# Kernel tuning notes

Measured on AMD Instinct MI355X. Metric: run time of the kernel, lower is better.

## Reference

```python
import math
import jax, jax.numpy as jnp
import numpy as np

B, LD, LE = 8, 512, 512
D, H, DK, F, L, V = 1024, 16, 64, 4096, 3, 32000
EPS = 1e-5
NEG = -1000000000.0


def setup_inputs() -> dict:
    key = jax.random.key(0)
    ks = jax.random.split(key, 16)
    s = 0.02
    dec_inputs = jax.random.randint(ks[0], (B, LD), 0, V)
    # causal mask: True = masked out (matches masked_fill semantics)
    self_mask = jnp.broadcast_to(jnp.triu(jnp.ones((LD, LD), bool), k=1), (B, LD, LD))
    enc_output = jax.random.normal(ks[1], (B, LE, D), jnp.float32)
    encoder_mask = jnp.zeros((B, LD, LE), bool)  # no encoder padding
    embed = jax.random.normal(ks[2], (V, D), jnp.float32) * s
    # sinusoidal positional encoding, pe[:LD]
    pos = jnp.arange(LD, dtype=jnp.float32)[:, None]
    div = jnp.exp(jnp.arange(0, D, 2, dtype=jnp.float32) * (-math.log(10000.0) / D))
    pe = jnp.zeros((LD, D), jnp.float32)
    pe = pe.at[:, 0::2].set(jnp.sin(pos * div)).at[:, 1::2].set(jnp.cos(pos * div))
    # per-layer params; axis 1 of attn params: 0=self-attn, 1=enc-dec attn
    wq = jax.random.normal(ks[3], (L, 2, D, D), jnp.float32) * s
    wk = jax.random.normal(ks[4], (L, 2, D, D), jnp.float32) * s
    wv = jax.random.normal(ks[5], (L, 2, D, D), jnp.float32) * s
    wo = jax.random.normal(ks[6], (L, 2, D, D), jnp.float32) * s
    bq = jnp.zeros((L, 2, D), jnp.float32)
    bk = jnp.zeros((L, 2, D), jnp.float32)
    bv = jnp.zeros((L, 2, D), jnp.float32)
    bo = jnp.zeros((L, 2, D), jnp.float32)
    ffn_w1 = jax.random.normal(ks[7], (L, F, D), jnp.float32) * s
    ffn_b1 = jnp.zeros((L, F), jnp.float32)
    ffn_w2 = jax.random.normal(ks[8], (L, D, F), jnp.float32) * s
    ffn_b2 = jnp.zeros((L, D), jnp.float32)
    ln_g = jnp.ones((L, 3, D), jnp.float32)   # norm1/2/3 gains
    ln_b = jnp.zeros((L, 3, D), jnp.float32)  # norm1/2/3 biases
    return dict(dec_inputs=dec_inputs, self_mask=self_mask, enc_output=enc_output,
                encoder_mask=encoder_mask, embed=embed, pe=pe,
                wq=wq, bq=bq, wk=wk, bk=bk, wv=wv, bv=bv, wo=wo, bo=bo,
                ffn_w1=ffn_w1, ffn_b1=ffn_b1, ffn_w2=ffn_w2, ffn_b2=ffn_b2,
                ln_g=ln_g, ln_b=ln_b)


def _ln(x, g, b):
    m = jnp.mean(x, axis=-1, keepdims=True)
    v = jnp.mean((x - m) ** 2, axis=-1, keepdims=True)
    return (x - m) * jax.lax.rsqrt(v + EPS) * g + b


def _mha(qi, ki, vi, mask, wq, bq, wk, bk, wv, bv, wo, bo):
    Bq, Lq, _ = qi.shape
    Lk = ki.shape[1]
    Q = (qi @ wq.T + bq).reshape(Bq, Lq, H, DK).transpose(0, 2, 1, 3)
    K = (ki @ wk.T + bk).reshape(Bq, Lk, H, DK).transpose(0, 2, 1, 3)
    Vv = (vi @ wv.T + bv).reshape(Bq, Lk, H, DK).transpose(0, 2, 1, 3)
    scores = jnp.einsum('bhqd,bhkd->bhqk', Q, K) / math.sqrt(DK)
    scores = jnp.where(mask[:, None, :, :], NEG, scores)
    attn = jax.nn.softmax(scores, axis=-1)
    ctx = jnp.einsum('bhqk,bhkd->bhqd', attn, Vv)
    ctx = ctx.transpose(0, 2, 1, 3).reshape(Bq, Lq, H * DK)
    return ctx @ wo.T + bo


def reference(dec_inputs, self_mask, enc_output, encoder_mask, embed, pe,
              wq, bq, wk, bk, wv, bv, wo, bo,
              ffn_w1, ffn_b1, ffn_w2, ffn_b2, ln_g, ln_b):
    x = embed[dec_inputs] * math.sqrt(D) + pe[None, :, :]
    for l in range(L):
        h = _ln(x, ln_g[l, 0], ln_b[l, 0])
        a = _mha(h, h, h, self_mask,
                 wq[l, 0], bq[l, 0], wk[l, 0], bk[l, 0], wv[l, 0], bv[l, 0], wo[l, 0], bo[l, 0])
        x = x + a
        h = _ln(x, ln_g[l, 1], ln_b[l, 1])
        c = _mha(h, enc_output, enc_output, encoder_mask,
                 wq[l, 1], bq[l, 1], wk[l, 1], bk[l, 1], wv[l, 1], bv[l, 1], wo[l, 1], bo[l, 1])
        x = x + c
        h = _ln(x, ln_g[l, 2], ln_b[l, 2])
        f = jax.nn.relu(h @ ffn_w1[l].T + ffn_b1[l]) @ ffn_w2[l].T + ffn_b2[l]
        # faithful quirk of the source: residual is the cross-attn output, not x
        x = c + f
    return x
```

## Files before the change

### kernel.cpp

```cpp
#include <hip/hip_runtime.h>
#include <hip/hip_bf16.h>

using bf16x8 = __attribute__((ext_vector_type(8))) short;
using f32x4  = __attribute__((ext_vector_type(4))) float;
using u16x4  = __attribute__((ext_vector_type(4))) unsigned short;

#define DEVI static __device__ __forceinline__

DEVI unsigned short f2b(float f) {
  unsigned int u = __float_as_uint(f);
  u += 0x7FFFu + ((u >> 16) & 1u);
  return (unsigned short)(u >> 16);
}

DEVI void gload16(const unsigned short* g, unsigned short* l) {
  __builtin_amdgcn_global_load_lds(
      (const __attribute__((address_space(1))) unsigned int*)g,
      (__attribute__((address_space(3))) unsigned int*)l, 16, 0, 0);
}

DEVI float wred_max16(float v) {
#pragma unroll
  for (int m = 1; m < 16; m <<= 1) v = fmaxf(v, __shfl_xor(v, m, 64));
  return v;
}
DEVI float wred_sum16(float v) {
#pragma unroll
  for (int m = 1; m < 16; m <<= 1) v += __shfl_xor(v, m, 64);
  return v;
}


__global__ void cvt_kernel(const float* __restrict__ in,
                           unsigned short* __restrict__ out, int n4) {
  int i = blockIdx.x * blockDim.x + threadIdx.x;
  const int stride = gridDim.x * blockDim.x;
  for (; i < n4; i += stride) {
    const float4 v = ((const float4*)in)[i];
    u16x4 o;
    o[0] = f2b(v.x); o[1] = f2b(v.y); o[2] = f2b(v.z); o[3] = f2b(v.w);
    ((u16x4*)out)[i] = o;
  }
}

__global__ void pack_w(const float* __restrict__ s0,
                       const float* __restrict__ s1,
                       const float* __restrict__ s2,
                       int sub, unsigned short* __restrict__ dst, int nm) {
  const int r = blockIdx.x;
  const int m = blockIdx.y;
  const int l = blockIdx.z;
  const float* src = (m == 0 ? s0 : m == 1 ? s1 : s2)
                   + (size_t)(l * 2 + sub) * 1048576 + (size_t)r * 1024;
  unsigned short* d = dst + ((size_t)(l * nm + m) * 1024 + r) * 1024;
  const int col = threadIdx.x * 4;
  const float4 v = *(const float4*)(src + col);
  u16x4 o;
  o[0] = f2b(v.x); o[1] = f2b(v.y); o[2] = f2b(v.z); o[3] = f2b(v.w);
  *(u16x4*)(d + col) = o;
}

__global__ void pack_bias(const float* __restrict__ s0,
                          const float* __restrict__ s1,
                          const float* __restrict__ s2,
                          int sub, float* __restrict__ dst, int nm) {
  const int m = blockIdx.x, l = blockIdx.y;
  const float* src = (m == 0 ? s0 : m == 1 ? s1 : s2) + (size_t)(l * 2 + sub) * 1024;
  float* d = dst + ((size_t)l * nm + m) * 1024;
  const int i = threadIdx.x * 4;
  *(float4*)(d + i) = *(const float4*)(src + i);
}

__global__ void embed_kernel(const int* __restrict__ ids,
                             const float* __restrict__ emb,
                             const float* __restrict__ pe,
                             float* __restrict__ x) {
  const int row = blockIdx.x;
  const int t = row & 511;
  const int col = threadIdx.x * 4;
  const int id = ids[row];
  const float4 e = *(const float4*)(emb + (size_t)id * 1024 + col);
  const float4 p = *(const float4*)(pe + (size_t)t * 1024 + col);
  float4 o;
  o.x = e.x * 32.f + p.x; o.y = e.y * 32.f + p.y;
  o.z = e.z * 32.f + p.z; o.w = e.w * 32.f + p.w;
  *(float4*)(x + (size_t)row * 1024 + col) = o;
}

__global__ void ln_kernel(const float* __restrict__ x,
                          const float* __restrict__ g,
                          const float* __restrict__ b,
                          unsigned short* __restrict__ out) {
  const int row = blockIdx.x;
  const int l = threadIdx.x;
  const float4* xr = (const float4*)(x + (size_t)row * 1024);
  float4 v[4];
  float s = 0.f;
#pragma unroll
  for (int i = 0; i < 4; ++i) {
    v[i] = xr[l * 4 + i];
    s += v[i].x + v[i].y + v[i].z + v[i].w;
  }
#pragma unroll
  for (int m = 1; m < 64; m <<= 1) s += __shfl_xor(s, m, 64);
  const float mean = s * (1.f / 1024.f);
  float vs = 0.f;
#pragma unroll
  for (int i = 0; i < 4; ++i) {
    float dx = v[i].x - mean, dy = v[i].y - mean, dz = v[i].z - mean, dw = v[i].w - mean;
    vs += dx * dx + dy * dy + dz * dz + dw * dw;
  }
#pragma unroll
  for (int m = 1; m < 64; m <<= 1) vs += __shfl_xor(vs, m, 64);
  const float inv = rsqrtf(vs * (1.f / 1024.f) + 1e-5f);
#pragma unroll
  for (int i = 0; i < 4; ++i) {
    const int col = l * 16 + i * 4;
    const float4 gg = *(const float4*)(g + col);
    const float4 bb = *(const float4*)(b + col);
    u16x4 o;
    o[0] = f2b((v[i].x - mean) * inv * gg.x + bb.x);
    o[1] = f2b((v[i].y - mean) * inv * gg.y + bb.y);
    o[2] = f2b((v[i].z - mean) * inv * gg.z + bb.z);
    o[3] = f2b((v[i].w - mean) * inv * gg.w + bb.w);
    *(u16x4*)(out + (size_t)row * 1024 + col) = o;
  }
}

__global__ void vt_kernel(const unsigned short* __restrict__ Vsrc, int vsd,
                          unsigned short* __restrict__ Vt) {
  __shared__ alignas(16) unsigned short t[64][72];
  const int tt = blockIdx.x;
  const int h  = blockIdx.y;
  const int b  = blockIdx.z;
  const int tid = threadIdx.x;
  const int r  = tid >> 2;
  const int ch = tid & 3;
  const unsigned short* src =
      Vsrc + (size_t)(b * 512 + tt * 64 + r) * vsd + (size_t)h * 64 + ch * 16;
  const bf16x8 v0 = *(const bf16x8*)src;
  const bf16x8 v1 = *(const bf16x8*)(src + 8);
#pragma unroll
  for (int j = 0; j < 8; ++j) {
    t[ch * 16 + j][r]     = (unsigned short)v0[j];
    t[ch * 16 + 8 + j][r] = (unsigned short)v1[j];
  }
  __syncthreads();
  const int d  = tid >> 2;
  const int tp = tid & 3;
  unsigned short* dst = Vt + (((size_t)(b * 16 + h) * 64 + d) * 512) + tt * 64 + tp * 16;
  *(bf16x8*)dst       = *(const bf16x8*)&t[d][tp * 16];
  *(bf16x8*)(dst + 8) = *(const bf16x8*)&t[d][tp * 16 + 8];
}


template<int EPI>
__global__ __launch_bounds__(512, 2) void gemm256(
    const unsigned short* __restrict__ A,
    const unsigned short* __restrict__ Bw,
    const float* __restrict__ bias,
    int N, unsigned short* __restrict__ out0) {
  constexpr int K = 1024, NK = 16;
  __shared__ alignas(16) unsigned short As0[256 * 64];
  __shared__ alignas(16) unsigned short As1[256 * 64];
  __shared__ alignas(16) unsigned short As2[256 * 64];
  __shared__ alignas(16) unsigned short Bs0[128 * 64];
  __shared__ alignas(16) unsigned short Bs1[128 * 64];
  __shared__ alignas(16) unsigned short Bs2[128 * 64];
  const int tid = threadIdx.x;
  const int lane = tid & 63;
  const int wave = tid >> 6;
  const int wr = wave >> 2;
  const int wc = wave & 3;
  int id = blockIdx.x;
  const int nwg = gridDim.x;
  id = (id & 7) * (nwg >> 3) + (id >> 3);
  const int nn = N >> 7;
  const int bx = id % nn;
  const int by = id / nn;
  const int m0 = by * 256;
  const int n0 = bx * 128;
  const int ro = lane & 15;
  const int hi = lane >> 4;

  auto stageA = [&](unsigned short* dst, int kt) {
    const size_t k0 = (size_t)kt * 64;
#pragma unroll
    for (int i = 0; i < 4; ++i) {
      const int c = tid + 512 * i;
      const int row = c >> 3;
      const int lc = (c & 7) ^ (row & 7);
      gload16(A + (size_t)(m0 + row) * K + k0 + lc * 8, dst + c * 8);
    }
  };
  auto stageB = [&](unsigned short* dst, int kt) {
    const size_t k0 = (size_t)kt * 64;
#pragma unroll
    for (int i = 0; i < 2; ++i) {
      const int c = tid + 512 * i;
      const int row = c >> 3;
      const int lc = (c & 7) ^ (row & 7);
      gload16(Bw + (size_t)(n0 + row) * K + k0 + lc * 8, dst + c * 8);
    }
  };

  f32x4 acc[8][2];
#pragma unroll
  for (int i = 0; i < 8; ++i)
#pragma unroll
    for (int j = 0; j < 2; ++j) acc[i][j] = f32x4{0.f, 0.f, 0.f, 0.f};

  stageA(As0, 0); stageB(Bs0, 0);
  stageA(As1, 1); stageB(Bs1, 1);

  auto body = [&](int kt, const unsigned short* Ac, const unsigned short* Bc,
                  unsigned short* An, unsigned short* Bn, bool last) {
    if (last) asm volatile("s_waitcnt vmcnt(0)" ::: "memory");
    else      asm volatile("s_waitcnt vmcnt(6)" ::: "memory");
    __builtin_amdgcn_s_barrier();
    if (kt + 2 < NK) { stageA(An, kt + 2); stageB(Bn, kt + 2); }
    bf16x8 af[8][2], bf[2][2];
#pragma unroll
    for (int mi = 0; mi < 8; ++mi) {
      const int r = wr * 128 + mi * 16 + ro;
#pragma unroll
      for (int ks = 0; ks < 2; ++ks)
        af[mi][ks] = *(const bf16x8*)&Ac[r * 64 + (((ks << 2) + hi) ^ (r & 7)) * 8];
    }
#pragma unroll
    for (int nj = 0; nj < 2; ++nj) {
      const int r = wc * 32 + nj * 16 + ro;
#pragma unroll
      for (int ks = 0; ks < 2; ++ks)
        bf[nj][ks] = *(const bf16x8*)&Bc[r * 64 + (((ks << 2) + hi) ^ (r & 7)) * 8];
    }
    __builtin_amdgcn_s_setprio(1);
#pragma unroll
    for (int ks = 0; ks < 2; ++ks)
#pragma unroll
      for (int mi = 0; mi < 8; ++mi)
#pragma unroll
        for (int nj = 0; nj < 2; ++nj)
          acc[mi][nj] = __builtin_amdgcn_mfma_f32_16x16x32_bf16(af[mi][ks], bf[nj][ks], acc[mi][nj], 0, 0, 0);
    __builtin_amdgcn_s_setprio(0);
  };

  for (int base = 0; base < 15; base += 3) {
    body(base,     As0, Bs0, As2, Bs2, false);
    body(base + 1, As1, Bs1, As0, Bs0, false);
    body(base + 2, As2, Bs2, As1, Bs1, false);
  }
  body(15, As0, Bs0, As1, Bs1, true);

  const int r4 = hi * 4;
#pragma unroll
  for (int mi = 0; mi < 8; ++mi) {
#pragma unroll
    for (int nj = 0; nj < 2; ++nj) {
      const int cg = n0 + wc * 32 + nj * 16 + ro;
      const float bv = bias[cg];
#pragma unroll
      for (int q = 0; q < 4; ++q) {
        const int rg = m0 + wr * 128 + mi * 16 + r4 + q;
        const float v = acc[mi][nj][q] + bv;
        out0[(size_t)rg * N + cg] = f2b(EPI == 1 ? fmaxf(v, 0.f) : v);
      }
    }
  }
}


enum { EPI_BF16 = 0, EPI_RELU_BF16 = 1, EPI_RES = 2, EPI_RES2 = 3 };

template<int EPI, int BM, int BN>
__global__ void gemm_bt(const unsigned short* __restrict__ A,
                        const unsigned short* __restrict__ Bw,
                        const float* __restrict__ bias,
                        int N, int K, int nn,
                        void* out0, const float* res, float* out1) {
  constexpr int MI = BM / 32;
  constexpr int NJ = BN / 32;
  __shared__ alignas(16) unsigned short As[2][BM * 64];
  __shared__ alignas(16) unsigned short Bs[2][BN * 64];
  const int tid = threadIdx.x;
  const int lane = tid & 63;
  const int wave = tid >> 6;
  int id = blockIdx.x;
  const int nwg = gridDim.x;
  id = (id & 7) * (nwg >> 3) + (id >> 3);
  const int bx = id % nn;
  const int by = id / nn;
  const int m0 = by * BM;
  const int n0 = bx * BN;
  const int wm = (wave >> 1) * (BM / 2);
  const int wn = (wave & 1) * (BN / 2);

  auto stage = [&](int buf, int kt) {
    const size_t k0 = (size_t)kt * 64;
#pragma unroll
    for (int i = 0; i < MI; ++i) {
      const int c = tid + 256 * i;
      const int row = c >> 3;
      const int lc = (c & 7) ^ (row & 7);
      gload16(A + (size_t)(m0 + row) * K + k0 + lc * 8, &As[buf][c * 8]);
    }
#pragma unroll
    for (int i = 0; i < NJ; ++i) {
      const int c = tid + 256 * i;
      const int row = c >> 3;
      const int lc = (c & 7) ^ (row & 7);
      gload16(Bw + (size_t)(n0 + row) * K + k0 + lc * 8, &Bs[buf][c * 8]);
    }
  };

  f32x4 acc[MI][NJ];
#pragma unroll
  for (int i = 0; i < MI; ++i)
#pragma unroll
    for (int j = 0; j < NJ; ++j) acc[i][j] = f32x4{0.f, 0.f, 0.f, 0.f};

  const int nk = K >> 6;
  stage(0, 0);
  int cur = 0;
  const int ro = lane & 15;
  const int hi = lane >> 4;
  for (int kt = 0; kt < nk; ++kt) {
    __syncthreads();
    if (kt + 1 < nk) stage(cur ^ 1, kt + 1);
    bf16x8 af[MI][2], bf[NJ][2];
#pragma unroll
    for (int i = 0; i < MI; ++i) {
      const int r = wm + i * 16 + ro;
#pragma unroll
      for (int ks = 0; ks < 2; ++ks)
        af[i][ks] = *(const bf16x8*)&As[cur][r * 64 + (((ks << 2) + hi) ^ (r & 7)) * 8];
    }
#pragma unroll
    for (int j = 0; j < NJ; ++j) {
      const int r = wn + j * 16 + ro;
#pragma unroll
      for (int ks = 0; ks < 2; ++ks)
        bf[j][ks] = *(const bf16x8*)&Bs[cur][r * 64 + (((ks << 2) + hi) ^ (r & 7)) * 8];
    }
#pragma unroll
    for (int ks = 0; ks < 2; ++ks)
#pragma unroll
      for (int i = 0; i < MI; ++i)
#pragma unroll
        for (int j = 0; j < NJ; ++j)
          acc[i][j] = __builtin_amdgcn_mfma_f32_16x16x32_bf16(af[i][ks], bf[j][ks], acc[i][j], 0, 0, 0);
    cur ^= 1;
  }

  const int r4 = hi * 4;
#pragma unroll
  for (int i = 0; i < MI; ++i) {
#pragma unroll
    for (int j = 0; j < NJ; ++j) {
      const int cg = n0 + wn + j * 16 + ro;
      const float bv = bias[cg];
#pragma unroll
      for (int q = 0; q < 4; ++q) {
        const int rg = m0 + wm + i * 16 + r4 + q;
        const size_t idx = (size_t)rg * N + cg;
        const float v = acc[i][j][q] + bv;
        if (EPI == EPI_BF16) {
          ((unsigned short*)out0)[idx] = f2b(v);
        } else if (EPI == EPI_RELU_BF16) {
          ((unsigned short*)out0)[idx] = f2b(fmaxf(v, 0.f));
        } else if (EPI == EPI_RES) {
          ((float*)out0)[idx] = res[idx] + v;
        } else {
          const float r = res[idx];
          ((float*)out0)[idx] = v;
          out1[idx] = r + v;
        }
      }
    }
  }
}


template<bool CAUSAL>
__global__ __launch_bounds__(64) void attn_kernel(
    const unsigned short* __restrict__ Qg, int qs,
    const unsigned short* __restrict__ Kg, int ksd,
    const unsigned short* __restrict__ Vt,
    unsigned short* __restrict__ Og) {
  __shared__ alignas(16) unsigned short Pl[32 * 64];
  const int qt = blockIdx.x;
  const int h  = blockIdx.y;
  const int b  = blockIdx.z;
  const int lane = threadIdx.x;
  const int ro = lane & 15;
  const int hi = lane >> 4;
  const size_t qbase = (size_t)b * 512 * qs  + (size_t)h * 64;
  const size_t kbase = (size_t)b * 512 * ksd + (size_t)h * 64;
  const size_t vbase = ((size_t)(b * 16 + h)) * 64 * 512;
  const size_t obase = (size_t)b * 512 * 1024 + (size_t)h * 64;

  bf16x8 qf[2][2];
#pragma unroll
  for (int mi = 0; mi < 2; ++mi)
#pragma unroll
    for (int ks = 0; ks < 2; ++ks)
      qf[mi][ks] = *(const bf16x8*)&Qg[qbase + (size_t)(qt * 32 + mi * 16 + ro) * qs + ks * 32 + hi * 8];

  f32x4 o[2][4];
  float mrun[2][4], lrun[2][4];
#pragma unroll
  for (int mi = 0; mi < 2; ++mi) {
#pragma unroll
    for (int di = 0; di < 4; ++di) o[mi][di] = f32x4{0.f, 0.f, 0.f, 0.f};
#pragma unroll
    for (int q = 0; q < 4; ++q) { mrun[mi][q] = -1e30f; lrun[mi][q] = 0.f; }
  }

  const int ktmax = CAUSAL ? (qt >> 1) : 7;
  for (int kt = 0; kt <= ktmax; ++kt) {
    bf16x8 kf[4][2];
#pragma unroll
    for (int ni = 0; ni < 4; ++ni)
#pragma unroll
      for (int ks = 0; ks < 2; ++ks)
        kf[ni][ks] = *(const bf16x8*)&Kg[kbase + (size_t)(kt * 64 + ni * 16 + ro) * ksd + ks * 32 + hi * 8];

    f32x4 s[2][4];
#pragma unroll
    for (int mi = 0; mi < 2; ++mi)
#pragma unroll
      for (int ni = 0; ni < 4; ++ni) s[mi][ni] = f32x4{0.f, 0.f, 0.f, 0.f};
#pragma unroll
    for (int ks = 0; ks < 2; ++ks)
#pragma unroll
      for (int mi = 0; mi < 2; ++mi)
#pragma unroll
        for (int ni = 0; ni < 4; ++ni)
          s[mi][ni] = __builtin_amdgcn_mfma_f32_16x16x32_bf16(qf[mi][ks], kf[ni][ks], s[mi][ni], 0, 0, 0);

#pragma unroll
    for (int mi = 0; mi < 2; ++mi)
#pragma unroll
      for (int ni = 0; ni < 4; ++ni)
#pragma unroll
        for (int q = 0; q < 4; ++q) {
          float e = s[mi][ni][q] * 0.125f;
          if (CAUSAL && kt == ktmax &&
              (kt * 64 + ni * 16 + ro) > (qt * 32 + mi * 16 + hi * 4 + q)) e = -1e9f;
          s[mi][ni][q] = e;
        }

    float fac[2][4];
#pragma unroll
    for (int mi = 0; mi < 2; ++mi)
#pragma unroll
      for (int q = 0; q < 4; ++q) {
        float rm = s[mi][0][q];
#pragma unroll
        for (int ni = 1; ni < 4; ++ni) rm = fmaxf(rm, s[mi][ni][q]);
        rm = wred_max16(rm);
        const float mn = fmaxf(mrun[mi][q], rm);
        fac[mi][q] = __expf(mrun[mi][q] - mn);
        mrun[mi][q] = mn;
      }
#pragma unroll
    for (int mi = 0; mi < 2; ++mi)
#pragma unroll
      for (int q = 0; q < 4; ++q) {
        float rs = 0.f;
#pragma unroll
        for (int ni = 0; ni < 4; ++ni) {
          const float pv = __expf(s[mi][ni][q] - mrun[mi][q]);
          s[mi][ni][q] = pv;
          rs += pv;
        }
        rs = wred_sum16(rs);
        lrun[mi][q] = lrun[mi][q] * fac[mi][q] + rs;
      }
#pragma unroll
    for (int mi = 0; mi < 2; ++mi)
#pragma unroll
      for (int di = 0; di < 4; ++di)
#pragma unroll
        for (int q = 0; q < 4; ++q) o[mi][di][q] *= fac[mi][q];

#pragma unroll
    for (int mi = 0; mi < 2; ++mi)
#pragma unroll
      for (int ni = 0; ni < 4; ++ni)
#pragma unroll
        for (int q = 0; q < 4; ++q) {
          const int row = mi * 16 + hi * 4 + q;
          const int col = ni * 16 + ro;
          const int sc  = ((col >> 3) ^ (row & 7)) * 8 + (col & 7);
          Pl[row * 64 + sc] = f2b(s[mi][ni][q]);
        }

    bf16x8 pa[2][2];
#pragma unroll
    for (int mi = 0; mi < 2; ++mi)
#pragma unroll
      for (int ks = 0; ks < 2; ++ks) {
        const int row = mi * 16 + ro;
        pa[mi][ks] = *(const bf16x8*)&Pl[row * 64 + (((ks << 2) + hi) ^ (row & 7)) * 8];
      }

#pragma unroll
    for (int di = 0; di < 4; ++di)
#pragma unroll
      for (int ks = 0; ks < 2; ++ks) {
        const bf16x8 vf = *(const bf16x8*)&Vt[vbase + (size_t)(di * 16 + ro) * 512 + kt * 64 + ks * 32 + hi * 8];
#pragma unroll
        for (int mi = 0; mi < 2; ++mi)
          o[mi][di] = __builtin_amdgcn_mfma_f32_16x16x32_bf16(pa[mi][ks], vf, o[mi][di], 0, 0, 0);
      }
  }

#pragma unroll
  for (int mi = 0; mi < 2; ++mi)
#pragma unroll
    for (int di = 0; di < 4; ++di)
#pragma unroll
      for (int q = 0; q < 4; ++q) {
        const float val = o[mi][di][q] / lrun[mi][q];
        Og[obase + (size_t)(qt * 32 + mi * 16 + hi * 4 + q) * 1024 + di * 16 + ro] = f2b(val);
      }
}


extern "C" void kernel_launch(void* const* d_in, const int* in_sizes, int n_in,
                              void* d_out, int out_size, void* d_ws, size_t ws_size,
                              hipStream_t stream) {
  (void)in_sizes; (void)n_in; (void)out_size; (void)ws_size;
  const int*   dec = (const int*)d_in[0];
  const float* enc = (const float*)d_in[2];
  const float* emb = (const float*)d_in[4];
  const float* pe  = (const float*)d_in[5];
  const float* wq  = (const float*)d_in[6];
  const float* bq  = (const float*)d_in[7];
  const float* wk  = (const float*)d_in[8];
  const float* bk  = (const float*)d_in[9];
  const float* wv  = (const float*)d_in[10];
  const float* bv  = (const float*)d_in[11];
  const float* wo  = (const float*)d_in[12];
  const float* bo  = (const float*)d_in[13];
  const float* w1  = (const float*)d_in[14];
  const float* b1  = (const float*)d_in[15];
  const float* w2  = (const float*)d_in[16];
  const float* b2  = (const float*)d_in[17];
  const float* lng = (const float*)d_in[18];
  const float* lnb = (const float*)d_in[19];

  const size_t SZ_ACT = 4194304ull;

  char* p = (char*)d_ws;
  auto alloc = [&](size_t bytes) { char* r = p; p += (bytes + 255) & ~(size_t)255; return r; };
  unsigned short* qkvw  = (unsigned short*)alloc(3ull * 3 * 1048576 * 2);
  unsigned short* kvw   = (unsigned short*)alloc(3ull * 2 * 1048576 * 2);
  unsigned short* wqxb  = (unsigned short*)alloc(3ull * 1048576 * 2);
  unsigned short* Wob   = (unsigned short*)alloc(6291456ull * 2);
  unsigned short* W1b   = (unsigned short*)alloc(12582912ull * 2);
  unsigned short* W2b   = (unsigned short*)alloc(12582912ull * 2);
  unsigned short* encb  = (unsigned short*)alloc(SZ_ACT * 2);
  float*          x     = (float*)alloc(SZ_ACT * 4);
  float*          c     = (float*)alloc(SZ_ACT * 4);
  unsigned short* hb    = (unsigned short*)alloc(SZ_ACT * 2);
  unsigned short* qkvb  = (unsigned short*)alloc(4096ull * 3072 * 2);
  unsigned short* kvb   = (unsigned short*)alloc(4096ull * 6144 * 2);
  unsigned short* qb    = (unsigned short*)alloc(SZ_ACT * 2);
  unsigned short* vtb   = (unsigned short*)alloc(SZ_ACT * 2);
  unsigned short* mid   = (unsigned short*)alloc(4096ull * 4096 * 2);
  float*          qkvbias = (float*)alloc(3ull * 3072 * 4);
  float*          kvbias  = (float*)alloc(3ull * 2048 * 4);

  cvt_kernel<<<2048, 256, 0, stream>>>(wo, Wob, 1572864);
  cvt_kernel<<<2048, 256, 0, stream>>>(w1, W1b, 3145728);
  cvt_kernel<<<2048, 256, 0, stream>>>(w2, W2b, 3145728);
  cvt_kernel<<<2048, 256, 0, stream>>>(enc, encb, 1048576);
  pack_w<<<dim3(1024, 3, 3), 256, 0, stream>>>(wq, wk, wv, 0, qkvw, 3);
  pack_w<<<dim3(1024, 2, 3), 256, 0, stream>>>(wk, wv, wv, 1, kvw, 2);
  pack_w<<<dim3(1024, 1, 3), 256, 0, stream>>>(wq, wq, wq, 1, wqxb, 1);
  pack_bias<<<dim3(3, 3), 256, 0, stream>>>(bq, bk, bv, 0, qkvbias, 3);
  pack_bias<<<dim3(2, 3), 256, 0, stream>>>(bk, bv, bv, 1, kvbias, 2);
  embed_kernel<<<4096, 256, 0, stream>>>(dec, emb, pe, x);

  gemm256<0><<<48 * 16, 512, 0, stream>>>(encb, kvw, kvbias, 6144, kvb);

  const dim3 gAttn(16, 16, 8);
  const dim3 gVt(8, 16, 8);

  for (int l = 0; l < 3; ++l) {
    const float* g0 = lng + (l * 3 + 0) * 1024; const float* e0 = lnb + (l * 3 + 0) * 1024;
    const float* g1 = lng + (l * 3 + 1) * 1024; const float* e1 = lnb + (l * 3 + 1) * 1024;
    const float* g2 = lng + (l * 3 + 2) * 1024; const float* e2 = lnb + (l * 3 + 2) * 1024;

    ln_kernel<<<4096, 64, 0, stream>>>(x, g0, e0, hb);
    gemm256<0><<<24 * 16, 512, 0, stream>>>(hb, qkvw + (size_t)l * 3 * 1048576,
        qkvbias + l * 3072, 3072, qkvb);
    vt_kernel<<<gVt, 256, 0, stream>>>(qkvb + 2048, 3072, vtb);
    attn_kernel<true><<<gAttn, 64, 0, stream>>>(qkvb, 3072, qkvb + 1024, 3072, vtb, hb);
    gemm_bt<EPI_RES, 128, 64><<<32 * 16, 256, 0, stream>>>(hb, Wob + (size_t)(l * 2) * 1048576,
        bo + (l * 2) * 1024, 1024, 1024, 16, x, x, nullptr);

    ln_kernel<<<4096, 64, 0, stream>>>(x, g1, e1, hb);
    gemm_bt<EPI_BF16, 128, 64><<<32 * 16, 256, 0, stream>>>(hb, wqxb + (size_t)l * 1048576,
        bq + (l * 2 + 1) * 1024, 1024, 1024, 16, qb, nullptr, nullptr);
    vt_kernel<<<gVt, 256, 0, stream>>>(kvb + l * 2048 + 1024, 6144, vtb);
    attn_kernel<false><<<gAttn, 64, 0, stream>>>(qb, 1024, kvb + l * 2048, 6144, vtb, hb);
    gemm_bt<EPI_RES2, 128, 64><<<32 * 16, 256, 0, stream>>>(hb, Wob + (size_t)(l * 2 + 1) * 1048576,
        bo + (l * 2 + 1) * 1024, 1024, 1024, 16, c, x, x);

    ln_kernel<<<4096, 64, 0, stream>>>(x, g2, e2, hb);
    gemm256<1><<<32 * 16, 512, 0, stream>>>(hb, W1b + (size_t)l * 4194304,
        b1 + l * 4096, 4096, mid);
    float* xout = (l == 2) ? (float*)d_out : x;
    gemm_bt<EPI_RES, 128, 64><<<32 * 16, 256, 0, stream>>>(mid, W2b + (size_t)l * 4194304,
        b2 + l * 1024, 1024, 4096, 16, xout, c, nullptr);
  }
}
```

Measured before the change: 1.183 ms.

## Share K/V tiles across four waves via double-buffered LDS staging in attention

The attention kernel now runs four waves per block, each owning 32 query rows of a 128-row tile. K and V tiles are loaded once per block into LDS with async global-to-LDS loads, double-buffered so the next tile is fetched while the current one is computed, and swizzled to avoid bank conflicts. This replaces per-wave direct global reads of K/V and cuts redundant memory traffic by 4x. In exchange the grid has fewer blocks, each iteration needs a barrier, and in the causal case the waves in a block have uneven work and the ones that finish early sit idle at the barriers.

```diff
diff --git a/kernel.cpp b/kernel.cpp
--- a/kernel.cpp
+++ b/kernel.cpp
@@ -382,18 +382,23 @@
 
 
 template<bool CAUSAL>
-__global__ __launch_bounds__(64) void attn_kernel(
+__global__ __launch_bounds__(256) void attn_kernel(
     const unsigned short* __restrict__ Qg, int qs,
     const unsigned short* __restrict__ Kg, int ksd,
     const unsigned short* __restrict__ Vt,
     unsigned short* __restrict__ Og) {
-  __shared__ alignas(16) unsigned short Pl[32 * 64];
-  const int qt = blockIdx.x;
+  __shared__ alignas(16) unsigned short Ks[2][64 * 64];
+  __shared__ alignas(16) unsigned short Vs[2][64 * 64];
+  __shared__ alignas(16) unsigned short Pl[4][32 * 64];
+  const int qt0 = blockIdx.x;
   const int h  = blockIdx.y;
   const int b  = blockIdx.z;
-  const int lane = threadIdx.x;
+  const int tid = threadIdx.x;
+  const int lane = tid & 63;
+  const int w = tid >> 6;
   const int ro = lane & 15;
   const int hi = lane >> 4;
+  const int qrow0 = qt0 * 128 + w * 32;
   const size_t qbase = (size_t)b * 512 * qs  + (size_t)h * 64;
   const size_t kbase = (size_t)b * 512 * ksd + (size_t)h * 64;
   const size_t vbase = ((size_t)(b * 16 + h)) * 64 * 512;
@@ -404,7 +409,7 @@
   for (int mi = 0; mi < 2; ++mi)
 #pragma unroll
     for (int ks = 0; ks < 2; ++ks)
-      qf[mi][ks] = *(const bf16x8*)&Qg[qbase + (size_t)(qt * 32 + mi * 16 + ro) * qs + ks * 32 + hi * 8];
+      qf[mi][ks] = *(const bf16x8*)&Qg[qbase + (size_t)(qrow0 + mi * 16 + ro) * qs + ks * 32 + hi * 8];
 
   f32x4 o[2][4];
   float mrun[2][4], lrun[2][4];
@@ -416,104 +421,132 @@
     for (int q = 0; q < 4; ++q) { mrun[mi][q] = -1e30f; lrun[mi][q] = 0.f; }
   }
 
-  const int ktmax = CAUSAL ? (qt >> 1) : 7;
+  auto stage = [&](int buf, int kt) {
+#pragma unroll
+    for (int i = 0; i < 2; ++i) {
+      const int c = tid + 256 * i;
+      const int row = c >> 3;
+      const int lc = (c & 7) ^ (row & 7);
+      gload16(Kg + kbase + (size_t)(kt * 64 + row) * ksd + lc * 8, &Ks[buf][c * 8]);
+    }
+#pragma unroll
+    for (int i = 0; i < 2; ++i) {
+      const int c = tid + 256 * i;
+      const int row = c >> 3;
+      const int lc = (c & 7) ^ (row & 7);
+      gload16(Vt + vbase + (size_t)row * 512 + (size_t)kt * 64 + lc * 8, &Vs[buf][c * 8]);
+    }
+  };
+
+  const int ktmax = CAUSAL ? (qt0 * 2 + 1) : 7;
+  stage(0, 0);
+  int cur = 0;
   for (int kt = 0; kt <= ktmax; ++kt) {
-    bf16x8 kf[4][2];
-#pragma unroll
-    for (int ni = 0; ni < 4; ++ni)
+    __syncthreads();
+    if (kt < ktmax) stage(cur ^ 1, kt + 1);
+    const bool skip = CAUSAL && (kt * 64 > qrow0 + 31);
+    if (!skip) {
+      bf16x8 kf[4][2];
+#pragma unroll
+      for (int ni = 0; ni < 4; ++ni) {
+        const int r = ni * 16 + ro;
+#pragma unroll
+        for (int ks = 0; ks < 2; ++ks)
+          kf[ni][ks] = *(const bf16x8*)&Ks[cur][r * 64 + (((ks << 2) + hi) ^ (r & 7)) * 8];
+      }
+
+      f32x4 s[2][4];
+#pragma unroll
+      for (int mi = 0; mi < 2; ++mi)
+#pragma unroll
+        for (int ni = 0; ni < 4; ++ni) s[mi][ni] = f32x4{0.f, 0.f, 0.f, 0.f};
 #pragma unroll
       for (int ks = 0; ks < 2; ++ks)
-        kf[ni][ks] = *(const bf16x8*)&Kg[kbase + (size_t)(kt * 64 + ni * 16 + ro) * ksd + ks * 32 + hi * 8];
-
-    f32x4 s[2][4];
-#pragma unroll
-    for (int mi = 0; mi < 2; ++mi)
-#pragma unroll
-      for (int ni = 0; ni < 4; ++ni) s[mi][ni] = f32x4{0.f, 0.f, 0.f, 0.f};
-#pragma unroll
-    for (int ks = 0; ks < 2; ++ks)
+#pragma unroll
+        for (int mi = 0; mi < 2; ++mi)
+#pragma unroll
+          for (int ni = 0; ni < 4; ++ni)
+            s[mi][ni] = __builtin_amdgcn_mfma_f32_16x16x32_bf16(qf[mi][ks], kf[ni][ks], s[mi][ni], 0, 0, 0);
+
+      const bool dm = CAUSAL && (kt * 64 + 63 > qrow0);
 #pragma unroll
       for (int mi = 0; mi < 2; ++mi)
 #pragma unroll
         for (int ni = 0; ni < 4; ++ni)
-          s[mi][ni] = __builtin_amdgcn_mfma_f32_16x16x32_bf16(qf[mi][ks], kf[ni][ks], s[mi][ni], 0, 0, 0);
-
-#pragma unroll
-    for (int mi = 0; mi < 2; ++mi)
-#pragma unroll
-      for (int ni = 0; ni < 4; ++ni)
+#pragma unroll
+          for (int q = 0; q < 4; ++q) {
+            float e = s[mi][ni][q] * 0.125f;
+            if (dm && (kt * 64 + ni * 16 + ro) > (qrow0 + mi * 16 + hi * 4 + q)) e = -1e9f;
+            s[mi][ni][q] = e;
+          }
+
+      float fac[2][4];
+#pragma unroll
+      for (int mi = 0; mi < 2; ++mi)
 #pragma unroll
         for (int q = 0; q < 4; ++q) {
-          float e = s[mi][ni][q] * 0.125f;
-          if (CAUSAL && kt == ktmax &&
-              (kt * 64 + ni * 16 + ro) > (qt * 32 + mi * 16 + hi * 4 + q)) e = -1e9f;
-          s[mi][ni][q] = e;
+          float rm = s[mi][0][q];
+#pragma unroll
+          for (int ni = 1; ni < 4; ++ni) rm = fmaxf(rm, s[mi][ni][q]);
+          rm = wred_max16(rm);
+          const float mn = fmaxf(mrun[mi][q], rm);
+          fac[mi][q] = __expf(mrun[mi][q] - mn);
+          mrun[mi][q] = mn;
         }
-
-    float fac[2][4];
-#pragma unroll
-    for (int mi = 0; mi < 2; ++mi)
-#pragma unroll
-      for (int q = 0; q < 4; ++q) {
-        float rm = s[mi][0][q];
-#pragma unroll
-        for (int ni = 1; ni < 4; ++ni) rm = fmaxf(rm, s[mi][ni][q]);
-        rm = wred_max16(rm);
-        const float mn = fmaxf(mrun[mi][q], rm);
-        fac[mi][q] = __expf(mrun[mi][q] - mn);
-        mrun[mi][q] = mn;
-      }
-#pragma unroll
-    for (int mi = 0; mi < 2; ++mi)
-#pragma unroll
-      for (int q = 0; q < 4; ++q) {
-        float rs = 0.f;
-#pragma unroll
-        for (int ni = 0; ni < 4; ++ni) {
-          const float pv = __expf(s[mi][ni][q] - mrun[mi][q]);
-          s[mi][ni][q] = pv;
-          rs += pv;
+#pragma unroll
+      for (int mi = 0; mi < 2; ++mi)
+#pragma unroll
+        for (int q = 0; q < 4; ++q) {
+          float rs = 0.f;
+#pragma unroll
+          for (int ni = 0; ni < 4; ++ni) {
+            const float pv = __expf(s[mi][ni][q] - mrun[mi][q]);
+            s[mi][ni][q] = pv;
+            rs += pv;
+          }
+          rs = wred_sum16(rs);
+          lrun[mi][q] = lrun[mi][q] * fac[mi][q] + rs;
         }
-        rs = wred_sum16(rs);
-        lrun[mi][q] = lrun[mi][q] * fac[mi][q] + rs;
-      }
-#pragma unroll
-    for (int mi = 0; mi < 2; ++mi)
+#pragma unroll
+      for (int mi = 0; mi < 2; ++mi)
+#pragma unroll
+        for (int di = 0; di < 4; ++di)
+#pragma unroll
+          for (int q = 0; q < 4; ++q) o[mi][di][q] *= fac[mi][q];
+
+#pragma unroll
+      for (int mi = 0; mi < 2; ++mi)
+#pragma unroll
+        for (int ni = 0; ni < 4; ++ni)
+#pragma unroll
+          for (int q = 0; q < 4; ++q) {
+            const int row = mi * 16 + hi * 4 + q;
+            const int col = ni * 16 + ro;
+            const int sc  = ((col >> 3) ^ (row & 7)) * 8 + (col & 7);
+            Pl[w][row * 64 + sc] = f2b(s[mi][ni][q]);
+          }
+
+      bf16x8 pa[2][2];
+#pragma unroll
+      for (int mi = 0; mi < 2; ++mi)
+#pragma unroll
+        for (int ks = 0; ks < 2; ++ks) {
+          const int row = mi * 16 + ro;
+          pa[mi][ks] = *(const bf16x8*)&Pl[w][row * 64 + (((ks << 2) + hi) ^ (row & 7)) * 8];
+        }
+
 #pragma unroll
       for (int di = 0; di < 4; ++di)
 #pragma unroll
-        for (int q = 0; q < 4; ++q) o[mi][di][q] *= fac[mi][q];
-
-#pragma unroll
-    for (int mi = 0; mi < 2; ++mi)
-#pragma unroll
-      for (int ni = 0; ni < 4; ++ni)
-#pragma unroll
-        for (int q = 0; q < 4; ++q) {
-          const int row = mi * 16 + hi * 4 + q;
-          const int col = ni * 16 + ro;
-          const int sc  = ((col >> 3) ^ (row & 7)) * 8 + (col & 7);
-          Pl[row * 64 + sc] = f2b(s[mi][ni][q]);
+        for (int ks = 0; ks < 2; ++ks) {
+          const int r = di * 16 + ro;
+          const bf16x8 vf = *(const bf16x8*)&Vs[cur][r * 64 + (((ks << 2) + hi) ^ (r & 7)) * 8];
+#pragma unroll
+          for (int mi = 0; mi < 2; ++mi)
+            o[mi][di] = __builtin_amdgcn_mfma_f32_16x16x32_bf16(pa[mi][ks], vf, o[mi][di], 0, 0, 0);
         }
-
-    bf16x8 pa[2][2];
-#pragma unroll
-    for (int mi = 0; mi < 2; ++mi)
-#pragma unroll
-      for (int ks = 0; ks < 2; ++ks) {
-        const int row = mi * 16 + ro;
-        pa[mi][ks] = *(const bf16x8*)&Pl[row * 64 + (((ks << 2) + hi) ^ (row & 7)) * 8];
-      }
-
-#pragma unroll
-    for (int di = 0; di < 4; ++di)
-#pragma unroll
-      for (int ks = 0; ks < 2; ++ks) {
-        const bf16x8 vf = *(const bf16x8*)&Vt[vbase + (size_t)(di * 16 + ro) * 512 + kt * 64 + ks * 32 + hi * 8];
-#pragma unroll
-        for (int mi = 0; mi < 2; ++mi)
-          o[mi][di] = __builtin_amdgcn_mfma_f32_16x16x32_bf16(pa[mi][ks], vf, o[mi][di], 0, 0, 0);
-      }
+    }
+    cur ^= 1;
   }
 
 #pragma unroll
@@ -523,7 +556,7 @@
 #pragma unroll
       for (int q = 0; q < 4; ++q) {
         const float val = o[mi][di][q] / lrun[mi][q];
-        Og[obase + (size_t)(qt * 32 + mi * 16 + hi * 4 + q) * 1024 + di * 16 + ro] = f2b(val);
+        Og[obase + (size_t)(qrow0 + mi * 16 + hi * 4 + q) * 1024 + di * 16 + ro] = f2b(val);
       }
 }
 
@@ -586,7 +619,7 @@
 
   gemm256<0><<<48 * 16, 512, 0, stream>>>(encb, kvw, kvbias, 6144, kvb);
 
-  const dim3 gAttn(16, 16, 8);
+  const dim3 gAttn(4, 16, 8);
   const dim3 gVt(8, 16, 8);
 
   for (int l = 0; l < 3; ++l) {
@@ -598,7 +631,7 @@
     gemm256<0><<<24 * 16, 512, 0, stream>>>(hb, qkvw + (size_t)l * 3 * 1048576,
         qkvbias + l * 3072, 3072, qkvb);
     vt_kernel<<<gVt, 256, 0, stream>>>(qkvb + 2048, 3072, vtb);
-    attn_kernel<true><<<gAttn, 64, 0, stream>>>(qkvb, 3072, qkvb + 1024, 3072, vtb, hb);
+    attn_kernel<true><<<gAttn, 256, 0, stream>>>(qkvb, 3072, qkvb + 1024, 3072, vtb, hb);
     gemm_bt<EPI_RES, 128, 64><<<32 * 16, 256, 0, stream>>>(hb, Wob + (size_t)(l * 2) * 1048576,
         bo + (l * 2) * 1024, 1024, 1024, 16, x, x, nullptr);
 
@@ -606,7 +639,7 @@
     gemm_bt<EPI_BF16, 128, 64><<<32 * 16, 256, 0, stream>>>(hb, wqxb + (size_t)l * 1048576,
         bq + (l * 2 + 1) * 1024, 1024, 1024, 16, qb, nullptr, nullptr);
     vt_kernel<<<gVt, 256, 0, stream>>>(kvb + l * 2048 + 1024, 6144, vtb);
-    attn_kernel<false><<<gAttn, 64, 0, stream>>>(qb, 1024, kvb + l * 2048, 6144, vtb, hb);
+    attn_kernel<false><<<gAttn, 256, 0, stream>>>(qb, 1024, kvb + l * 2048, 6144, vtb, hb);
     gemm_bt<EPI_RES2, 128, 64><<<32 * 16, 256, 0, stream>>>(hb, Wob + (size_t)(l * 2 + 1) * 1048576,
         bo + (l * 2 + 1) * 1024, 1024, 1024, 16, c, x, x);
 
```

Result: faster. 1.140 ms (-3.6%).
